# Kernel optimization log

Measured on AMD Instinct MI355X. Metric: run time of the kernel, lower is better.

Reference implementation:

```python
import jax, jax.numpy as jnp
import numpy as np

N = 100000          # nodes (src == target here)
E = 1600000         # edges, avg degree 16
C_IN = 128
C_OUT = 128
R = 7               # num_edge_types
T = 4               # num_node_types


def setup_inputs() -> dict:
    key = jax.random.key(0)
    ks = jax.random.split(key, 7)
    x = jax.random.normal(ks[0], (N, C_IN), dtype=jnp.float32)
    edge_index = jax.random.randint(ks[1], (2, E), 0, N, dtype=jnp.int32)
    edge_type = jax.random.randint(ks[2], (E,), 0, R, dtype=jnp.int32)
    target_node_type = jax.random.randint(ks[3], (N,), 0, T, dtype=jnp.int32)
    # Linear weights: rel_lins (no bias), root_lins (with bias); torch Linear: y = x @ W.T + b
    rel_w = jax.random.normal(ks[4], (R, C_OUT, C_IN), dtype=jnp.float32) * (1.0 / np.sqrt(C_IN))
    root_w = jax.random.normal(ks[5], (T, C_OUT, C_IN), dtype=jnp.float32) * (1.0 / np.sqrt(C_IN))
    root_b = jax.random.normal(ks[6], (T, C_OUT), dtype=jnp.float32) * 0.01
    return {"x": x, "edge_index": edge_index, "edge_type": edge_type,
            "target_node_type": target_node_type,
            "rel_w": rel_w, "root_w": root_w, "root_b": root_b}


def reference(x, edge_index, edge_type, target_node_type, rel_w, root_w, root_b):
    # Per-edge-type gather -> (bias-free) linear -> scatter-mean.
    # linear commutes with mean (no bias), so aggregate first, then apply W_r.
    n = x.shape[0]
    src, dst = edge_index[0], edge_index[1]
    x_j = x[src]                                   # [E, C_in] gather
    seg = dst.astype(jnp.int32) * R + edge_type    # fused (node, edge_type) segment id
    sums = jax.ops.segment_sum(x_j, seg, num_segments=n * R).reshape(n, R, C_IN)
    cnt = jax.ops.segment_sum(jnp.ones((x_j.shape[0],), x.dtype), seg,
                              num_segments=n * R).reshape(n, R)
    means = sums / jnp.maximum(cnt, 1.0)[:, :, None]   # zero rows stay zero (PyG mean of empty = 0)
    out = jnp.einsum('nrc,roc->no', means, rel_w)       # sum_r rel_lins[r](mean_r)
    # Per-node-type root linear with bias (small loop over T=4 types).
    for t in range(T):
        m = (target_node_type == t).astype(x.dtype)[:, None]
        out = out + m * (x @ root_w[t].T + root_b[t])
    return out
```

## Files before the change

kernel.cpp:

```cpp
#include <hip/hip_runtime.h>

#define N_NODES 100000
#define N_EDGES 1600000
#define C_DIM   128
#define R_TYPES 7
#define T_TYPES 4
#define SEGS    (N_NODES * R_TYPES)
#define NB_E    (N_EDGES / 256)
#define NB_N    ((N_NODES + 255) / 256)
#define XP_ROWS 100096
#define DST_PART 12500

#define OFF_CNTI   0ull
#define OFF_INV    2800000ull
#define OFF_DOFF   5600000ull
#define OFF_CURS   6000004ull
#define OFF_MISC   6400004ull
#define OFF_PERM   6400132ull
#define PERM_CAP   100288
#define N_PERM_BLOCKS 1567
#define OFF_BLKN   6801284ull
#define OFF_BSUM   6813796ull
#define OFF_ESRC   6815360ull
#define OFF_XP     13215360ull
#define OFF_WF     38839936ull
#define OFF_XWB    39069312ull
#define XWB_PLANE  ((size_t)XP_ROWS * 128)
#define FULL_NEED  218441344ull
#define FB_NEED    64693888ull

typedef __attribute__((ext_vector_type(8))) short short8;
typedef __attribute__((ext_vector_type(4))) float f32x4;

__device__ inline unsigned short f2bf(float f) {
    unsigned int u = __float_as_uint(f);
    u += 0x7fffu + ((u >> 16) & 1u);
    return (unsigned short)(u >> 16);
}
__device__ inline float bf2f(unsigned int h) { return __uint_as_float(h << 16); }

__global__ void edge_hist(const int* __restrict__ ei, const int* __restrict__ et,
                          int* __restrict__ cnti) {
    int e = blockIdx.x * 256 + threadIdx.x;
    atomicAdd(&cnti[ei[N_EDGES + e] * R_TYPES + et[e]], 1);
}

__global__ void inv_kernel(const int* __restrict__ cnti, float* __restrict__ inv) {
    int i = blockIdx.x * blockDim.x + threadIdx.x;
    if (i < SEGS) inv[i] = 1.0f / (float)max(cnti[i], 1);
}

__global__ void dst_scan1(const int* __restrict__ cnti, int* __restrict__ dst_off,
                          int* __restrict__ bsum) {
    __shared__ int sbuf[256];
    int tid = threadIdx.x;
    int i = blockIdx.x * 256 + tid;
    int v = 0;
    if (i < N_NODES) {
        #pragma unroll
        for (int r = 0; r < R_TYPES; ++r) v += cnti[i * R_TYPES + r];
    }
    sbuf[tid] = v;
    __syncthreads();
    #pragma unroll
    for (int off = 1; off < 256; off <<= 1) {
        int t = (tid >= off) ? sbuf[tid - off] : 0;
        __syncthreads();
        sbuf[tid] += t;
        __syncthreads();
    }
    int incl = sbuf[tid];
    if (i < N_NODES) dst_off[i] = incl - v;
    if (tid == 255) bsum[blockIdx.x] = incl;
}

__global__ void seg_scan2(int* __restrict__ bsum, int nb) {
    __shared__ int sbuf[256];
    int tid = threadIdx.x;
    int running = 0;
    for (int c0 = 0; c0 < nb; c0 += 256) {
        int b = c0 + tid;
        int v = (b < nb) ? bsum[b] : 0;
        sbuf[tid] = v;
        __syncthreads();
        #pragma unroll
        for (int off = 1; off < 256; off <<= 1) {
            int t = (tid >= off) ? sbuf[tid - off] : 0;
            __syncthreads();
            sbuf[tid] += t;
            __syncthreads();
        }
        int incl = sbuf[tid];
        int tot = sbuf[255];
        __syncthreads();
        if (b < nb) bsum[b] = running + incl - v;
        running += tot;
    }
}

__global__ void dst_scan3(int* __restrict__ dst_off, int* __restrict__ cursor,
                          const int* __restrict__ bsum) {
    int i = blockIdx.x * 256 + threadIdx.x;
    if (i < N_NODES) {
        int val = dst_off[i] + bsum[blockIdx.x];
        dst_off[i] = val;
        cursor[i] = val;
    }
    if (i == 0) dst_off[N_NODES] = N_EDGES;
}

__global__ void place_edges(const int* __restrict__ ei, const int* __restrict__ et,
                            int* __restrict__ cursor, int* __restrict__ esrc) {
    int p = blockIdx.x & 7;
    int e = (blockIdx.x >> 3) * 256 + threadIdx.x;
    int d = ei[N_EDGES + e];
    if (d / DST_PART != p) return;
    int pos = atomicAdd(&cursor[d], 1);
    esrc[pos] = (et[e] << 17) | ei[e];
}

__global__ void node_hist(const int* __restrict__ tnt, int* __restrict__ blk_n) {
    __shared__ int h[8];
    int tid = threadIdx.x;
    if (tid < 8) h[tid] = 0;
    __syncthreads();
    int n = blockIdx.x * 256 + tid;
    if (n < N_NODES) atomicAdd(&h[tnt[n]], 1);
    __syncthreads();
    if (tid < T_TYPES) blk_n[blockIdx.x * 8 + tid] = h[tid];
}

__global__ void scan_blocks(int* __restrict__ blk, int nb, int* __restrict__ total) {
    __shared__ int sbuf[256];
    int r = blockIdx.x;
    int tid = threadIdx.x;
    int running = 0;
    for (int c0 = 0; c0 < nb; c0 += 256) {
        int b = c0 + tid;
        int v = (b < nb) ? blk[b * 8 + r] : 0;
        sbuf[tid] = v;
        __syncthreads();
        #pragma unroll
        for (int off = 1; off < 256; off <<= 1) {
            int t = (tid >= off) ? sbuf[tid - off] : 0;
            __syncthreads();
            sbuf[tid] += t;
            __syncthreads();
        }
        int incl = sbuf[tid];
        int chunk_total = sbuf[255];
        __syncthreads();
        if (b < nb) blk[b * 8 + r] = running + incl - v;
        running += chunk_total;
    }
    if (tid == 0) total[r] = running;
}

__global__ void offsets_kernel(int* misc) {
    if (threadIdx.x == 0 && blockIdx.x == 0) {
        int s = 0;
        for (int t = 0; t < T_TYPES; ++t) {
            misc[4 + t] = s;
            s += ((misc[t] + 63) / 64) * 64;
        }
    }
}

__global__ void node_scatter(const int* __restrict__ tnt, const int* __restrict__ misc,
                             const int* __restrict__ blk_n, int* __restrict__ perm) {
    __shared__ int h[8];
    int tid = threadIdx.x;
    if (tid < 8) h[tid] = 0;
    __syncthreads();
    int n = blockIdx.x * 256 + tid;
    if (n < N_NODES) {
        int t = tnt[n];
        int rank = atomicAdd(&h[t], 1);
        perm[misc[4 + t] + blk_n[blockIdx.x * 8 + t] + rank] = n;
    }
}

__global__ void cvt_x_frag(const float* __restrict__ x, unsigned short* __restrict__ xp) {
    int id = blockIdx.x * 256 + threadIdx.x;
    int n = id >> 4, ko = id & 15;
    short8 o;
    if (n < N_NODES) {
        const float4* px = (const float4*)(x + (size_t)n * C_DIM + ko * 8);
        float4 a = px[0], b = px[1];
        o[0] = (short)f2bf(a.x); o[1] = (short)f2bf(a.y);
        o[2] = (short)f2bf(a.z); o[3] = (short)f2bf(a.w);
        o[4] = (short)f2bf(b.x); o[5] = (short)f2bf(b.y);
        o[6] = (short)f2bf(b.z); o[7] = (short)f2bf(b.w);
    } else {
        o = (short8)0;
    }
    size_t off = (size_t)(n >> 4) * 2048 + (ko >> 2) * 512 + (ko & 3) * 128 + (n & 15) * 8;
    *(short8*)(xp + off) = o;
}

__global__ void cvt_w_frag(const float* __restrict__ rel_w, unsigned short* __restrict__ wf) {
    int id = blockIdx.x * 256 + threadIdx.x;
    if (id >= R_TYPES * 128 * 16) return;
    int r = id >> 11, rest = id & 2047;
    int o = rest >> 4, ko = rest & 15;
    const float4* pw = (const float4*)(rel_w + (size_t)r * 16384 + o * 128 + ko * 8);
    float4 a = pw[0], b = pw[1];
    short8 v;
    v[0] = (short)f2bf(a.x); v[1] = (short)f2bf(a.y);
    v[2] = (short)f2bf(a.z); v[3] = (short)f2bf(a.w);
    v[4] = (short)f2bf(b.x); v[5] = (short)f2bf(b.y);
    v[6] = (short)f2bf(b.z); v[7] = (short)f2bf(b.w);
    size_t off = (size_t)r * 16384 + (o >> 4) * 2048 + (ko >> 2) * 512 + (ko & 3) * 128 + (o & 15) * 8;
    *(short8*)(wf + off) = v;
}

__launch_bounds__(256)
__global__ void xw_gemm_all(const unsigned short* __restrict__ xp,
                            const unsigned short* __restrict__ wf,
                            unsigned short* __restrict__ xwb7) {
    int wave = threadIdx.x >> 6, lane = threadIdx.x & 63;
    int m0 = blockIdx.x * 128;

    short8 a[4][2];
    #pragma unroll
    for (int kb = 0; kb < 4; ++kb)
        #pragma unroll
        for (int rt = 0; rt < 2; ++rt) {
            size_t rtile = (size_t)blockIdx.x * 8 + wave * 2 + rt;
            a[kb][rt] = *(const short8*)(xp + rtile * 2048 + kb * 512 + lane * 8);
        }

    int col = lane & 15, rq = (lane >> 4) * 4;
    for (int r = 0; r < R_TYPES; ++r) {
        const unsigned short* wr = wf + (size_t)r * 16384;
        unsigned short* xwb = xwb7 + (size_t)r * XWB_PLANE;
        #pragma unroll
        for (int ct = 0; ct < 8; ++ct) {
            f32x4 acc0 = (f32x4)0.0f, acc1 = (f32x4)0.0f;
            #pragma unroll
            for (int kb = 0; kb < 4; ++kb) {
                short8 b = *(const short8*)(wr + (size_t)ct * 2048 + kb * 512 + lane * 8);
                acc0 = __builtin_amdgcn_mfma_f32_16x16x32_bf16(a[kb][0], b, acc0, 0, 0, 0);
                acc1 = __builtin_amdgcn_mfma_f32_16x16x32_bf16(a[kb][1], b, acc1, 0, 0, 0);
            }
            #pragma unroll
            for (int i = 0; i < 4; ++i) {
                int n0 = m0 + wave * 32 + rq + i;
                if (n0 < N_NODES)
                    xwb[(size_t)n0 * C_DIM + ct * 16 + col] = f2bf(acc0[i]);
                int n1 = n0 + 16;
                if (n1 < N_NODES)
                    xwb[(size_t)n1 * C_DIM + ct * 16 + col] = f2bf(acc1[i]);
            }
        }
    }
}

__launch_bounds__(256)
__global__ void xw_gemm_mfma(const unsigned short* __restrict__ xp,
                             const unsigned short* __restrict__ wf,
                             unsigned short* __restrict__ xwb, int r) {
    int wave = threadIdx.x >> 6, lane = threadIdx.x & 63;
    int m0 = blockIdx.x * 128;
    const unsigned short* wr = wf + (size_t)r * 16384;

    short8 a[4][2];
    #pragma unroll
    for (int kb = 0; kb < 4; ++kb)
        #pragma unroll
        for (int rt = 0; rt < 2; ++rt) {
            size_t rtile = (size_t)blockIdx.x * 8 + wave * 2 + rt;
            a[kb][rt] = *(const short8*)(xp + rtile * 2048 + kb * 512 + lane * 8);
        }

    int col = lane & 15, rq = (lane >> 4) * 4;
    #pragma unroll
    for (int ct = 0; ct < 8; ++ct) {
        f32x4 acc0 = (f32x4)0.0f, acc1 = (f32x4)0.0f;
        #pragma unroll
        for (int kb = 0; kb < 4; ++kb) {
            short8 b = *(const short8*)(wr + (size_t)ct * 2048 + kb * 512 + lane * 8);
            acc0 = __builtin_amdgcn_mfma_f32_16x16x32_bf16(a[kb][0], b, acc0, 0, 0, 0);
            acc1 = __builtin_amdgcn_mfma_f32_16x16x32_bf16(a[kb][1], b, acc1, 0, 0, 0);
        }
        #pragma unroll
        for (int i = 0; i < 4; ++i) {
            int n0 = m0 + wave * 32 + rq + i;
            if (n0 < N_NODES)
                xwb[(size_t)n0 * C_DIM + ct * 16 + col] = f2bf(acc0[i]);
            int n1 = n0 + 16;
            if (n1 < N_NODES)
                xwb[(size_t)n1 * C_DIM + ct * 16 + col] = f2bf(acc1[i]);
        }
    }
}

__global__ void gather_fused(const int* __restrict__ dst_off, const int* __restrict__ esrc,
                             const float* __restrict__ inv,
                             const unsigned short* __restrict__ xwb7,
                             float* __restrict__ out) {
    int wave = threadIdx.x >> 6, lane = threadIdx.x & 63;
    int d = blockIdx.x * 4 + wave;
    if (d >= N_NODES) return;
    int o0 = dst_off[d], o1 = dst_off[d + 1];
    float ax = 0.0f, ay = 0.0f;
    int pk_next = (o0 < o1) ? esrc[o0] : 0;
    for (int e = o0; e < o1; ++e) {
        int pk = pk_next;
        if (e + 1 < o1) pk_next = esrc[e + 1];
        int src = pk & 0x1ffff;
        int r   = pk >> 17;
        float sc = inv[d * R_TYPES + r];
        unsigned int row = *(const unsigned int*)(xwb7 + ((size_t)r * XP_ROWS + src) * C_DIM + lane * 2);
        ax += bf2f(row & 0xffffu) * sc;
        ay += bf2f(row >> 16) * sc;
    }
    float2* po = (float2*)(out + (size_t)d * C_DIM) + lane;
    *po = make_float2(ax, ay);
}

__global__ void gather_rel_f(const int* __restrict__ dst_off, const int* __restrict__ esrc,
                             const float* __restrict__ inv,
                             const unsigned short* __restrict__ xwb,
                             float* __restrict__ out, int rf) {
    int wave = threadIdx.x >> 6, lane = threadIdx.x & 63;
    int d = blockIdx.x * 4 + wave;
    if (d >= N_NODES) return;
    int o0 = dst_off[d], o1 = dst_off[d + 1];
    float ax = 0.0f, ay = 0.0f;
    bool any = false;
    for (int e = o0; e < o1; ++e) {
        int pk = esrc[e];
        if ((pk >> 17) != rf) continue;
        any = true;
        int src = pk & 0x1ffff;
        unsigned int row = *(const unsigned int*)(xwb + (size_t)src * C_DIM + lane * 2);
        ax += bf2f(row & 0xffffu);
        ay += bf2f(row >> 16);
    }
    if (!any) return;
    float sc = inv[d * R_TYPES + rf];
    float2* po = (float2*)(out + (size_t)d * C_DIM) + lane;
    float2 v = *po;
    v.x += ax * sc;
    v.y += ay * sc;
    *po = v;
}

#define ASTR 33
#define BSTR 132
__launch_bounds__(256, 2)
__global__ void root_gemm(const float* __restrict__ x, const float* __restrict__ root_w,
                          const float* __restrict__ root_b, const int* __restrict__ tnt,
                          const int* __restrict__ perm, float* __restrict__ out) {
    __shared__ int   pidx[64];
    __shared__ float As[64 * ASTR];
    __shared__ float Bs[32 * BSTR];
    int tid = threadIdx.x;
    if (tid < 64) pidx[tid] = perm[blockIdx.x * 64 + tid];
    __syncthreads();
    if (pidx[0] < 0) return;
    int t = tnt[pidx[0]];
    int tx = tid & 15;
    int ty = tid >> 4;
    float acc[4][8];
    #pragma unroll
    for (int i = 0; i < 4; ++i)
        #pragma unroll
        for (int j = 0; j < 8; ++j) acc[i][j] = 0.0f;

    for (int kb = 0; kb < 4; ++kb) {
        #pragma unroll
        for (int p = 0; p < 2; ++p) {
            int idx = p * 256 + tid;
            int row = idx >> 3;
            int cc  = (idx & 7) * 4;
            int node = pidx[row];
            float4 v = make_float4(0.f, 0.f, 0.f, 0.f);
            if (node >= 0)
                v = *(const float4*)(x + (size_t)node * C_DIM + kb * 32 + cc);
            As[row * ASTR + cc + 0] = v.x;
            As[row * ASTR + cc + 1] = v.y;
            As[row * ASTR + cc + 2] = v.z;
            As[row * ASTR + cc + 3] = v.w;
        }
        #pragma unroll
        for (int p = 0; p < 4; ++p) {
            int idx = p * 256 + tid;
            int o  = idx >> 3;
            int cc = (idx & 7) * 4;
            float4 v = *(const float4*)(root_w + ((size_t)t * 128 + o) * 128 + kb * 32 + cc);
            Bs[(cc + 0) * BSTR + o] = v.x;
            Bs[(cc + 1) * BSTR + o] = v.y;
            Bs[(cc + 2) * BSTR + o] = v.z;
            Bs[(cc + 3) * BSTR + o] = v.w;
        }
        __syncthreads();
        #pragma unroll
        for (int k = 0; k < 32; ++k) {
            float a[4];
            #pragma unroll
            for (int i = 0; i < 4; ++i) a[i] = As[(ty * 4 + i) * ASTR + k];
            float4 b0 = *(const float4*)&Bs[k * BSTR + tx * 4];
            float4 b1 = *(const float4*)&Bs[k * BSTR + 64 + tx * 4];
            float b[8] = {b0.x, b0.y, b0.z, b0.w, b1.x, b1.y, b1.z, b1.w};
            #pragma unroll
            for (int i = 0; i < 4; ++i)
                #pragma unroll
                for (int j = 0; j < 8; ++j) acc[i][j] += a[i] * b[j];
        }
        __syncthreads();
    }
    float4 bias0 = *(const float4*)(root_b + (size_t)t * 128 + tx * 4);
    float4 bias1 = *(const float4*)(root_b + (size_t)t * 128 + 64 + tx * 4);
    #pragma unroll
    for (int i = 0; i < 4; ++i) {
        int node = pidx[ty * 4 + i];
        if (node < 0) continue;
        float* po = out + (size_t)node * C_DIM;
        float4 v0 = *(float4*)(po + tx * 4);
        float4 v1 = *(float4*)(po + 64 + tx * 4);
        v0.x += acc[i][0] + bias0.x;  v0.y += acc[i][1] + bias0.y;
        v0.z += acc[i][2] + bias0.z;  v0.w += acc[i][3] + bias0.w;
        v1.x += acc[i][4] + bias1.x;  v1.y += acc[i][5] + bias1.y;
        v1.z += acc[i][6] + bias1.z;  v1.w += acc[i][7] + bias1.w;
        *(float4*)(po + tx * 4) = v0;
        *(float4*)(po + 64 + tx * 4) = v1;
    }
}

extern "C" void kernel_launch(void* const* d_in, const int* in_sizes, int n_in,
                              void* d_out, int out_size, void* d_ws, size_t ws_size,
                              hipStream_t stream) {
    const float* x      = (const float*)d_in[0];
    const int*   ei     = (const int*)d_in[1];
    const int*   et     = (const int*)d_in[2];
    const int*   tnt    = (const int*)d_in[3];
    const float* rel_w  = (const float*)d_in[4];
    const float* root_w = (const float*)d_in[5];
    const float* root_b = (const float*)d_in[6];
    float* out = (float*)d_out;

    char* ws = (char*)d_ws;
    int*   cnti    = (int*)(ws + OFF_CNTI);
    float* inv     = (float*)(ws + OFF_INV);
    int*   dst_off = (int*)(ws + OFF_DOFF);
    int*   cursor  = (int*)(ws + OFF_CURS);
    int*   misc    = (int*)(ws + OFF_MISC);
    int*   perm    = (int*)(ws + OFF_PERM);
    int*   blk_n   = (int*)(ws + OFF_BLKN);
    int*   bsum    = (int*)(ws + OFF_BSUM);
    int*   esrc    = (int*)(ws + OFF_ESRC);
    unsigned short* xp  = (unsigned short*)(ws + OFF_XP);
    unsigned short* wf  = (unsigned short*)(ws + OFF_WF);
    unsigned short* xwb = (unsigned short*)(ws + OFF_XWB);

    const bool full = (ws_size >= FULL_NEED);

    hipMemsetAsync(ws + OFF_CNTI, 0, SEGS * sizeof(int), stream);
    hipMemsetAsync(ws + OFF_MISC, 0, 32 * sizeof(int), stream);
    hipMemsetAsync(ws + OFF_PERM, 0xFF, (size_t)PERM_CAP * sizeof(int), stream);
    if (!full)
        hipMemsetAsync(d_out, 0, (size_t)out_size * sizeof(float), stream);

    edge_hist  <<<NB_E, 256, 0, stream>>>(ei, et, cnti);
    inv_kernel <<<(SEGS + 255) / 256, 256, 0, stream>>>(cnti, inv);
    dst_scan1  <<<NB_N, 256, 0, stream>>>(cnti, dst_off, bsum);
    seg_scan2  <<<1, 256, 0, stream>>>(bsum, NB_N);
    dst_scan3  <<<NB_N, 256, 0, stream>>>(dst_off, cursor, bsum);
    place_edges<<<NB_E * 8, 256, 0, stream>>>(ei, et, cursor, esrc);

    node_hist  <<<NB_N, 256, 0, stream>>>(tnt, blk_n);
    scan_blocks<<<T_TYPES, 256, 0, stream>>>(blk_n, NB_N, misc + 0);
    offsets_kernel<<<1, 64, 0, stream>>>(misc);
    node_scatter<<<NB_N, 256, 0, stream>>>(tnt, misc, blk_n, perm);

    cvt_x_frag<<<(XP_ROWS * 16) / 256, 256, 0, stream>>>(x, xp);
    cvt_w_frag<<<56, 256, 0, stream>>>(rel_w, wf);

    if (full) {
        xw_gemm_all <<<XP_ROWS / 128, 256, 0, stream>>>(xp, wf, xwb);
        gather_fused<<<(N_NODES + 3) / 4, 256, 0, stream>>>(dst_off, esrc, inv, xwb, out);
    } else {
        for (int r = 0; r < R_TYPES; ++r) {
            xw_gemm_mfma<<<XP_ROWS / 128, 256, 0, stream>>>(xp, wf, xwb, r);
            gather_rel_f<<<(N_NODES + 3) / 4, 256, 0, stream>>>(dst_off, esrc, inv, xwb, out, r);
        }
    }
    root_gemm<<<N_PERM_BLOCKS, 256, 0, stream>>>(x, root_w, root_b, tnt, perm, out);
}
```

Before: 533.3 us.

## Split wave into half-waves processing two edges each with 8-byte loads

The gather kernel now has each half-wave handle a different edge. Each lane loads 4 bf16 values (uint2) instead of 2, and the loop is unrolled so four edges are in flight per iteration. The two halves are combined with a cross-half shuffle before a float4 store. The packed edge word now holds the precomputed row index r*XP_ROWS+src in 20 bits with the type in the upper bits, which removes the per-edge multiply-add in the address math. This is meant to raise memory-level parallelism in the latency-bound gather, at the cost of a shuffle reduction and masked tail handling.

```diff
diff --git a/kernel.cpp b/kernel.cpp
--- a/kernel.cpp
+++ b/kernel.cpp
@@ -116,7 +116,8 @@
     int d = ei[N_EDGES + e];
     if (d / DST_PART != p) return;
     int pos = atomicAdd(&cursor[d], 1);
-    esrc[pos] = (et[e] << 17) | ei[e];
+    int r = et[e];
+    esrc[pos] = (r << 20) | (r * XP_ROWS + ei[e]);
 }
 
 __global__ void node_hist(const int* __restrict__ tnt, int* __restrict__ blk_n) {
@@ -303,20 +304,45 @@
     int d = blockIdx.x * 4 + wave;
     if (d >= N_NODES) return;
     int o0 = dst_off[d], o1 = dst_off[d + 1];
-    float ax = 0.0f, ay = 0.0f;
-    int pk_next = (o0 < o1) ? esrc[o0] : 0;
-    for (int e = o0; e < o1; ++e) {
-        int pk = pk_next;
-        if (e + 1 < o1) pk_next = esrc[e + 1];
-        int src = pk & 0x1ffff;
-        int r   = pk >> 17;
-        float sc = inv[d * R_TYPES + r];
-        unsigned int row = *(const unsigned int*)(xwb7 + ((size_t)r * XP_ROWS + src) * C_DIM + lane * 2);
-        ax += bf2f(row & 0xffffu) * sc;
-        ay += bf2f(row >> 16) * sc;
-    }
-    float2* po = (float2*)(out + (size_t)d * C_DIM) + lane;
-    *po = make_float2(ax, ay);
+    int half = lane >> 5;
+    int l32 = lane & 31;
+    const float* invd = inv + d * R_TYPES;
+    float a0 = 0.f, a1 = 0.f, a2 = 0.f, a3 = 0.f;
+
+    int e = o0;
+    for (; e + 4 <= o1; e += 4) {
+        int pkA = esrc[e + half];
+        int pkB = esrc[e + 2 + half];
+        const uint2* pA = (const uint2*)(xwb7 + (size_t)(pkA & 0xFFFFF) * C_DIM + l32 * 4);
+        const uint2* pB = (const uint2*)(xwb7 + (size_t)(pkB & 0xFFFFF) * C_DIM + l32 * 4);
+        uint2 rA = *pA;
+        uint2 rB = *pB;
+        float sA = invd[pkA >> 20];
+        float sB = invd[pkB >> 20];
+        a0 += bf2f(rA.x & 0xffffu) * sA;  a1 += bf2f(rA.x >> 16) * sA;
+        a2 += bf2f(rA.y & 0xffffu) * sA;  a3 += bf2f(rA.y >> 16) * sA;
+        a0 += bf2f(rB.x & 0xffffu) * sB;  a1 += bf2f(rB.x >> 16) * sB;
+        a2 += bf2f(rB.y & 0xffffu) * sB;  a3 += bf2f(rB.y >> 16) * sB;
+    }
+    for (; e < o1; e += 2) {
+        int idx = e + half;
+        bool valid = idx < o1;
+        int pk = esrc[valid ? idx : e];
+        const uint2* p = (const uint2*)(xwb7 + (size_t)(pk & 0xFFFFF) * C_DIM + l32 * 4);
+        uint2 rw = *p;
+        float s = valid ? invd[pk >> 20] : 0.0f;
+        a0 += bf2f(rw.x & 0xffffu) * s;  a1 += bf2f(rw.x >> 16) * s;
+        a2 += bf2f(rw.y & 0xffffu) * s;  a3 += bf2f(rw.y >> 16) * s;
+    }
+
+    a0 += __shfl_xor(a0, 32);
+    a1 += __shfl_xor(a1, 32);
+    a2 += __shfl_xor(a2, 32);
+    a3 += __shfl_xor(a3, 32);
+    if (lane < 32) {
+        float4 v = make_float4(a0, a1, a2, a3);
+        ((float4*)(out + (size_t)d * C_DIM))[lane] = v;
+    }
 }
 
 __global__ void gather_rel_f(const int* __restrict__ dst_off, const int* __restrict__ esrc,
@@ -331,9 +357,9 @@
     bool any = false;
     for (int e = o0; e < o1; ++e) {
         int pk = esrc[e];
-        if ((pk >> 17) != rf) continue;
+        if ((pk >> 20) != rf) continue;
         any = true;
-        int src = pk & 0x1ffff;
+        int src = (pk & 0xFFFFF) - rf * XP_ROWS;
         unsigned int row = *(const unsigned int*)(xwb + (size_t)src * C_DIM + lane * 2);
         ax += bf2f(row & 0xffffu);
         ay += bf2f(row >> 16);
```

Result: faster. 501.1 us (-6.0%).
